# Optimization experiments

Measured on AMD Instinct MI355X. Metric: run time of the kernel, lower is better.

Reference implementation:

```python
import jax, jax.numpy as jnp
import numpy as np

B = 16384
S = 7
CELL = 1.0 / 7.0   # CELL_SILE
LC = 5.0           # lambda_coord
LN = 0.5           # lambda_noobj


def setup_inputs() -> dict:
    key = jax.random.key(0)
    k1, k2, k3 = jax.random.split(key, 3)
    predictions = jax.random.normal(k1, (B, S, S, 30), dtype=jnp.float32)
    targets = jax.random.uniform(k2, (B, S, S, 30), dtype=jnp.float32)
    # channel 4 is the objectness flag; code requires it to be exactly 0 or 1
    conf = (jax.random.uniform(k3, (B, S, S)) < 0.25).astype(jnp.float32)
    targets = targets.at[..., 4].set(conf)
    return {"predictions": predictions, "targets": targets}


def _box_corners(xy, wh):
    # Faithful to the original in-place bug: x2y2 uses the ALREADY-UPDATED x1y1
    xy1 = xy * CELL - wh * 0.5
    xy2 = xy1 * CELL + wh * 0.5
    return xy1, xy2


def _loss_terms(predictions, targets):
    p = predictions.reshape(-1, 30)   # [N, 30], N = B*S*S
    t = targets.reshape(-1, 30)
    obj = (t[:, 4] == 1.0).astype(p.dtype)
    noobj = (t[:, 4] == 0.0).astype(p.dtype)

    # no-object confidence loss on cols 4 and 9
    noobj_loss = LN * jnp.sum(noobj * (jnp.square(p[:, 4] - t[:, 4]) + jnp.square(p[:, 9] - t[:, 9])))

    # two predicted boxes per cell: cols 0:4 and 5:9 ; wh are sqrt-encoded -> square
    pb = jnp.stack([p[:, 0:4], p[:, 5:9]], axis=1)        # [N, 2, 4]
    pxy1, pxy2 = _box_corners(pb[..., 0:2], jnp.square(pb[..., 2:4]))  # [N,2,2]
    txy1, txy2 = _box_corners(t[:, None, 0:2], jnp.square(t[:, None, 2:4]))  # [N,1,2]

    # torchvision.ops.box_iou math (no clamp on areas, clamp(0) on intersection)
    lt = jnp.maximum(pxy1, txy1)
    rb = jnp.minimum(pxy2, txy2)
    inter = jnp.prod(jnp.clip(rb - lt, 0.0, None), axis=-1)   # [N, 2]
    area_p = jnp.prod(pxy2 - pxy1, axis=-1)                   # [N, 2]
    area_t = jnp.prod(txy2 - txy1, axis=-1)                   # [N, 1]
    iou = inter / (area_p + area_t - inter)                   # [N, 2]

    idx = jnp.argmax(iou, axis=1)                             # responsible box in {0,1}

    cols = idx[:, None] * 5 + jnp.arange(4)[None, :]          # [N, 4]
    cp = jnp.take_along_axis(p, cols, axis=1)
    ct = jnp.take_along_axis(t, cols, axis=1)
    center_loss = LC * jnp.sum(obj * jnp.sum(jnp.square(cp[:, 0:2] - ct[:, 0:2]), axis=1))
    wh_loss = LC * jnp.sum(obj * jnp.sum(jnp.square(cp[:, 2:4] - ct[:, 2:4]), axis=1))

    ccol = (idx * 5 + 4)[:, None]
    conf_loss = LC * jnp.sum(obj * jnp.square(jnp.take_along_axis(p, ccol, axis=1) - jnp.take_along_axis(t, ccol, axis=1))[:, 0])

    kcol = (jnp.argmax(t[:, 10:30], axis=1) + 10)[:, None]
    cls_loss = LC * jnp.sum(obj * jnp.square(jnp.take_along_axis(p, kcol, axis=1) - jnp.take_along_axis(t, kcol, axis=1))[:, 0])

    total = noobj_loss + center_loss + wh_loss + conf_loss + cls_loss
    return cls_loss, conf_loss, center_loss + wh_loss, total


def reference(predictions, targets):
    return _loss_terms(predictions, targets)
```

## Files before the change

### kernel.cpp

```cpp
#include <hip/hip_runtime.h>


constexpr int   WSZ  = 64;
constexpr int   NC   = 16384 * 7 * 7;
constexpr int   NT   = NC / WSZ;
constexpr int   GRID = 4096;
constexpr float CELL = 1.0f / 7.0f;
constexpr float LC   = 5.0f;
constexpr float LN   = 0.5f;

__launch_bounds__(WSZ, 4)
__global__ void yolo_partial(const float* __restrict__ P, const float* __restrict__ T,
                             float4* __restrict__ ws)
{
    __shared__ float sT[WSZ * 30];
    const int lane = threadIdx.x;
    float a_cls = 0.f, a_conf = 0.f, a_cw = 0.f, a_noobj = 0.f;

    for (int tile = blockIdx.x; tile < NT; tile += GRID) {
        const size_t base = (size_t)tile * (WSZ * 30);

        const float4* gT = reinterpret_cast<const float4*>(T + base);
        float4* s4 = reinterpret_cast<float4*>(sT);
        #pragma unroll
        for (int k = 0; k < 8; ++k) {
            int idx = k * WSZ + lane;
            if (idx < 480) s4[idx] = gT[idx];
        }

        const float* prow = P + base + (size_t)lane * 30;
        float pv[10];
        #pragma unroll
        for (int j = 0; j < 5; ++j) {
            float2 v = reinterpret_cast<const float2*>(prow)[j];
            pv[2 * j] = v.x; pv[2 * j + 1] = v.y;
        }
        __syncthreads();

        const float* tt = sT + lane * 30;
        float tv[30];
        #pragma unroll
        for (int j = 0; j < 15; ++j) {
            float2 v = reinterpret_cast<const float2*>(tt)[j];
            tv[2 * j] = v.x; tv[2 * j + 1] = v.y;
        }

        int kc = 10;
        float best = tv[10];
        #pragma unroll
        for (int k = 11; k < 30; ++k) {
            if (tv[k] > best) { best = tv[k]; kc = k; }
        }
        float2 pg = *reinterpret_cast<const float2*>(prow + (kc & ~1));
        float pk = (kc & 1) ? pg.y : pg.x;

        const float t4 = tv[4];
        const float obj   = (t4 == 1.0f) ? 1.0f : 0.0f;
        const float noobj = (t4 == 0.0f) ? 1.0f : 0.0f;

        float d4 = pv[4] - t4;
        float d9 = pv[9] - tv[9];
        a_noobj += noobj * (d4 * d4 + d9 * d9);

        float tw2 = tv[2] * tv[2], th2 = tv[3] * tv[3];
        float tx1 = tv[0] * CELL - 0.5f * tw2;
        float tx2 = tx1 * CELL + 0.5f * tw2;
        float ty1 = tv[1] * CELL - 0.5f * th2;
        float ty2 = ty1 * CELL + 0.5f * th2;
        float area_t = (tx2 - tx1) * (ty2 - ty1);

        float iou0, iou1;
        #pragma unroll
        for (int b = 0; b < 2; ++b) {
            float bw2 = pv[5 * b + 2] * pv[5 * b + 2];
            float bh2 = pv[5 * b + 3] * pv[5 * b + 3];
            float px1 = pv[5 * b + 0] * CELL - 0.5f * bw2;
            float px2 = px1 * CELL + 0.5f * bw2;
            float py1 = pv[5 * b + 1] * CELL - 0.5f * bh2;
            float py2 = py1 * CELL + 0.5f * bh2;
            float ltx = fmaxf(px1, tx1), lty = fmaxf(py1, ty1);
            float rbx = fminf(px2, tx2), rby = fminf(py2, ty2);
            float inter = fmaxf(rbx - ltx, 0.0f) * fmaxf(rby - lty, 0.0f);
            float area_p = (px2 - px1) * (py2 - py1);
            float iou = inter / (area_p + area_t - inter);
            if (b == 0) iou0 = iou; else iou1 = iou;
        }
        const bool b1 = (iou1 > iou0);

        float cpx = b1 ? pv[5] : pv[0], ctx = b1 ? tv[5] : tv[0];
        float cpy = b1 ? pv[6] : pv[1], cty = b1 ? tv[6] : tv[1];
        float cpw = b1 ? pv[7] : pv[2], ctw = b1 ? tv[7] : tv[2];
        float cph = b1 ? pv[8] : pv[3], cth = b1 ? tv[8] : tv[3];
        float cpc = b1 ? pv[9] : pv[4], ctc = b1 ? tv[9] : tv[4];

        float dx = cpx - ctx, dy = cpy - cty;
        float dw = cpw - ctw, dh = cph - cth;
        a_cw   += obj * (dx * dx + dy * dy + dw * dw + dh * dh);
        float dc = cpc - ctc;
        a_conf += obj * dc * dc;
        float dk = pk - best;
        a_cls  += obj * dk * dk;

        __syncthreads();
    }

    float vals[4] = { a_cls, a_conf, a_cw, a_noobj };
    #pragma unroll
    for (int c = 0; c < 4; ++c) {
        #pragma unroll
        for (int off = 32; off > 0; off >>= 1)
            vals[c] += __shfl_down(vals[c], off, 64);
    }
    if (lane == 0)
        ws[blockIdx.x] = make_float4(vals[0], vals[1], vals[2], vals[3]);
}

__launch_bounds__(1024, 1)
__global__ void yolo_reduce(const float4* __restrict__ ws, float* __restrict__ out)
{
    __shared__ float red[4][16];
    const int tid = threadIdx.x;

    float s0 = 0.f, s1 = 0.f, s2 = 0.f, s3 = 0.f;
    for (int b = tid; b < GRID; b += 1024) {
        float4 v = ws[b];
        s0 += v.x; s1 += v.y; s2 += v.z; s3 += v.w;
    }
    float vals[4] = { s0, s1, s2, s3 };
    #pragma unroll
    for (int c = 0; c < 4; ++c) {
        #pragma unroll
        for (int off = 32; off > 0; off >>= 1)
            vals[c] += __shfl_down(vals[c], off, 64);
        if ((tid & 63) == 0) red[c][tid >> 6] = vals[c];
    }
    __syncthreads();
    if (tid == 0) {
        float t0 = 0.f, t1 = 0.f, t2 = 0.f, t3 = 0.f;
        #pragma unroll
        for (int w = 0; w < 16; ++w) {
            t0 += red[0][w]; t1 += red[1][w]; t2 += red[2][w]; t3 += red[3][w];
        }
        out[0] = LC * t0;
        out[1] = LC * t1;
        out[2] = LC * t2;
        out[3] = LN * t3 + LC * (t0 + t1 + t2);
    }
}

extern "C" void kernel_launch(void* const* d_in, const int* in_sizes, int n_in,
                              void* d_out, int out_size, void* d_ws, size_t ws_size,
                              hipStream_t stream) {
    const float* P = (const float*)d_in[0];
    const float* T = (const float*)d_in[1];
    float* out = (float*)d_out;
    float4* ws = (float4*)d_ws;

    yolo_partial<<<GRID, WSZ, 0, stream>>>(P, T, ws);
    yolo_reduce<<<1, 1024, 0, stream>>>(ws, out);
}
```

Measured before the change: 207.3 us.

## Load two cells per thread with float4 loads and drop shared-memory staging

```diff
diff --git a/kernel.cpp b/kernel.cpp
--- a/kernel.cpp
+++ b/kernel.cpp
@@ -1,108 +1,106 @@
 #include <hip/hip_runtime.h>
 
 
-constexpr int   WSZ  = 64;
-constexpr int   NC   = 16384 * 7 * 7;
-constexpr int   NT   = NC / WSZ;
-constexpr int   GRID = 4096;
-constexpr float CELL = 1.0f / 7.0f;
-constexpr float LC   = 5.0f;
-constexpr float LN   = 0.5f;
+constexpr int   TPB   = 256;
+constexpr int   NC    = 16384 * 7 * 7;
+constexpr int   NPAIR = NC / 2;
+constexpr int   NBLK  = NPAIR / TPB;
+constexpr float CELL  = 1.0f / 7.0f;
+constexpr float LC    = 5.0f;
+constexpr float LN    = 0.5f;
 
-__launch_bounds__(WSZ, 4)
+__device__ __forceinline__ void cell_terms(const float* __restrict__ pv,
+                                           const float* __restrict__ tv,
+                                           float& a_cls, float& a_conf,
+                                           float& a_cw, float& a_noobj)
+{
+    const float t4 = tv[4];
+    const float obj   = (t4 == 1.0f) ? 1.0f : 0.0f;
+    const float noobj = (t4 == 0.0f) ? 1.0f : 0.0f;
+
+    float d4 = pv[4] - t4;
+    float d9 = pv[9] - tv[9];
+    a_noobj += noobj * (d4 * d4 + d9 * d9);
+
+    float tw2 = tv[2] * tv[2], th2 = tv[3] * tv[3];
+    float tx1 = tv[0] * CELL - 0.5f * tw2;
+    float tx2 = tx1 * CELL + 0.5f * tw2;
+    float ty1 = tv[1] * CELL - 0.5f * th2;
+    float ty2 = ty1 * CELL + 0.5f * th2;
+    float area_t = (tx2 - tx1) * (ty2 - ty1);
+
+    float iou0, iou1;
+    #pragma unroll
+    for (int b = 0; b < 2; ++b) {
+        float bw2 = pv[5 * b + 2] * pv[5 * b + 2];
+        float bh2 = pv[5 * b + 3] * pv[5 * b + 3];
+        float px1 = pv[5 * b + 0] * CELL - 0.5f * bw2;
+        float px2 = px1 * CELL + 0.5f * bw2;
+        float py1 = pv[5 * b + 1] * CELL - 0.5f * bh2;
+        float py2 = py1 * CELL + 0.5f * bh2;
+        float ltx = fmaxf(px1, tx1), lty = fmaxf(py1, ty1);
+        float rbx = fminf(px2, tx2), rby = fminf(py2, ty2);
+        float inter = fmaxf(rbx - ltx, 0.0f) * fmaxf(rby - lty, 0.0f);
+        float area_p = (px2 - px1) * (py2 - py1);
+        float iou = inter / (area_p + area_t - inter);
+        if (b == 0) iou0 = iou; else iou1 = iou;
+    }
+    const bool b1 = (iou1 > iou0);
+
+    float cpx = b1 ? pv[5] : pv[0], ctx = b1 ? tv[5] : tv[0];
+    float cpy = b1 ? pv[6] : pv[1], cty = b1 ? tv[6] : tv[1];
+    float cpw = b1 ? pv[7] : pv[2], ctw = b1 ? tv[7] : tv[2];
+    float cph = b1 ? pv[8] : pv[3], cth = b1 ? tv[8] : tv[3];
+    float cpc = b1 ? pv[9] : pv[4], ctc = b1 ? tv[9] : tv[4];
+
+    float dx = cpx - ctx, dy = cpy - cty;
+    float dw = cpw - ctw, dh = cph - cth;
+    a_cw   += obj * (dx * dx + dy * dy + dw * dw + dh * dh);
+    float dc = cpc - ctc;
+    a_conf += obj * dc * dc;
+
+    float best = tv[10];
+    float pk   = pv[10];
+    #pragma unroll
+    for (int k = 11; k < 30; ++k) {
+        bool gt = (tv[k] > best);
+        best = gt ? tv[k] : best;
+        pk   = gt ? pv[k] : pk;
+    }
+    float dk = pk - best;
+    a_cls += obj * dk * dk;
+}
+
+__launch_bounds__(TPB, 2)
 __global__ void yolo_partial(const float* __restrict__ P, const float* __restrict__ T,
                              float4* __restrict__ ws)
 {
-    __shared__ float sT[WSZ * 30];
-    const int lane = threadIdx.x;
+    __shared__ float red[4][TPB / 64];
+
+    const int tid  = threadIdx.x;
+    const int pair = blockIdx.x * TPB + tid;
+
+    const float4* p4 = reinterpret_cast<const float4*>(P + (size_t)pair * 60);
+    const float4* t4 = reinterpret_cast<const float4*>(T + (size_t)pair * 60);
+
+    float4 pr[15], tr[15];
+    #pragma unroll
+    for (int j = 0; j < 15; ++j) pr[j] = p4[j];
+    #pragma unroll
+    for (int j = 0; j < 15; ++j) tr[j] = t4[j];
+
+    float pv[60], tv[60];
+    #pragma unroll
+    for (int j = 0; j < 15; ++j) {
+        pv[4 * j + 0] = pr[j].x; pv[4 * j + 1] = pr[j].y;
+        pv[4 * j + 2] = pr[j].z; pv[4 * j + 3] = pr[j].w;
+        tv[4 * j + 0] = tr[j].x; tv[4 * j + 1] = tr[j].y;
+        tv[4 * j + 2] = tr[j].z; tv[4 * j + 3] = tr[j].w;
+    }
+
     float a_cls = 0.f, a_conf = 0.f, a_cw = 0.f, a_noobj = 0.f;
-
-    for (int tile = blockIdx.x; tile < NT; tile += GRID) {
-        const size_t base = (size_t)tile * (WSZ * 30);
-
-        const float4* gT = reinterpret_cast<const float4*>(T + base);
-        float4* s4 = reinterpret_cast<float4*>(sT);
-        #pragma unroll
-        for (int k = 0; k < 8; ++k) {
-            int idx = k * WSZ + lane;
-            if (idx < 480) s4[idx] = gT[idx];
-        }
-
-        const float* prow = P + base + (size_t)lane * 30;
-        float pv[10];
-        #pragma unroll
-        for (int j = 0; j < 5; ++j) {
-            float2 v = reinterpret_cast<const float2*>(prow)[j];
-            pv[2 * j] = v.x; pv[2 * j + 1] = v.y;
-        }
-        __syncthreads();
-
-        const float* tt = sT + lane * 30;
-        float tv[30];
-        #pragma unroll
-        for (int j = 0; j < 15; ++j) {
-            float2 v = reinterpret_cast<const float2*>(tt)[j];
-            tv[2 * j] = v.x; tv[2 * j + 1] = v.y;
-        }
-
-        int kc = 10;
-        float best = tv[10];
-        #pragma unroll
-        for (int k = 11; k < 30; ++k) {
-            if (tv[k] > best) { best = tv[k]; kc = k; }
-        }
-        float2 pg = *reinterpret_cast<const float2*>(prow + (kc & ~1));
-        float pk = (kc & 1) ? pg.y : pg.x;
-
-        const float t4 = tv[4];
-        const float obj   = (t4 == 1.0f) ? 1.0f : 0.0f;
-        const float noobj = (t4 == 0.0f) ? 1.0f : 0.0f;
-
-        float d4 = pv[4] - t4;
-        float d9 = pv[9] - tv[9];
-        a_noobj += noobj * (d4 * d4 + d9 * d9);
-
-        float tw2 = tv[2] * tv[2], th2 = tv[3] * tv[3];
-        float tx1 = tv[0] * CELL - 0.5f * tw2;
-        float tx2 = tx1 * CELL + 0.5f * tw2;
-        float ty1 = tv[1] * CELL - 0.5f * th2;
-        float ty2 = ty1 * CELL + 0.5f * th2;
-        float area_t = (tx2 - tx1) * (ty2 - ty1);
-
-        float iou0, iou1;
-        #pragma unroll
-        for (int b = 0; b < 2; ++b) {
-            float bw2 = pv[5 * b + 2] * pv[5 * b + 2];
-            float bh2 = pv[5 * b + 3] * pv[5 * b + 3];
-            float px1 = pv[5 * b + 0] * CELL - 0.5f * bw2;
-            float px2 = px1 * CELL + 0.5f * bw2;
-            float py1 = pv[5 * b + 1] * CELL - 0.5f * bh2;
-            float py2 = py1 * CELL + 0.5f * bh2;
-            float ltx = fmaxf(px1, tx1), lty = fmaxf(py1, ty1);
-            float rbx = fminf(px2, tx2), rby = fminf(py2, ty2);
-            float inter = fmaxf(rbx - ltx, 0.0f) * fmaxf(rby - lty, 0.0f);
-            float area_p = (px2 - px1) * (py2 - py1);
-            float iou = inter / (area_p + area_t - inter);
-            if (b == 0) iou0 = iou; else iou1 = iou;
-        }
-        const bool b1 = (iou1 > iou0);
-
-        float cpx = b1 ? pv[5] : pv[0], ctx = b1 ? tv[5] : tv[0];
-        float cpy = b1 ? pv[6] : pv[1], cty = b1 ? tv[6] : tv[1];
-        float cpw = b1 ? pv[7] : pv[2], ctw = b1 ? tv[7] : tv[2];
-        float cph = b1 ? pv[8] : pv[3], cth = b1 ? tv[8] : tv[3];
-        float cpc = b1 ? pv[9] : pv[4], ctc = b1 ? tv[9] : tv[4];
-
-        float dx = cpx - ctx, dy = cpy - cty;
-        float dw = cpw - ctw, dh = cph - cth;
-        a_cw   += obj * (dx * dx + dy * dy + dw * dw + dh * dh);
-        float dc = cpc - ctc;
-        a_conf += obj * dc * dc;
-        float dk = pk - best;
-        a_cls  += obj * dk * dk;
-
-        __syncthreads();
-    }
+    cell_terms(pv,      tv,      a_cls, a_conf, a_cw, a_noobj);
+    cell_terms(pv + 30, tv + 30, a_cls, a_conf, a_cw, a_noobj);
 
     float vals[4] = { a_cls, a_conf, a_cw, a_noobj };
     #pragma unroll
@@ -110,9 +108,17 @@
         #pragma unroll
         for (int off = 32; off > 0; off >>= 1)
             vals[c] += __shfl_down(vals[c], off, 64);
+        if ((tid & 63) == 0) red[c][tid >> 6] = vals[c];
     }
-    if (lane == 0)
-        ws[blockIdx.x] = make_float4(vals[0], vals[1], vals[2], vals[3]);
+    __syncthreads();
+    if (tid == 0) {
+        float4 s;
+        s.x = red[0][0] + red[0][1] + red[0][2] + red[0][3];
+        s.y = red[1][0] + red[1][1] + red[1][2] + red[1][3];
+        s.z = red[2][0] + red[2][1] + red[2][2] + red[2][3];
+        s.w = red[3][0] + red[3][1] + red[3][2] + red[3][3];
+        ws[blockIdx.x] = s;
+    }
 }
 
 __launch_bounds__(1024, 1)
@@ -122,7 +128,7 @@
     const int tid = threadIdx.x;
 
     float s0 = 0.f, s1 = 0.f, s2 = 0.f, s3 = 0.f;
-    for (int b = tid; b < GRID; b += 1024) {
+    for (int b = tid; b < NBLK; b += 1024) {
         float4 v = ws[b];
         s0 += v.x; s1 += v.y; s2 += v.z; s3 += v.w;
     }
@@ -156,6 +162,6 @@
     float* out = (float*)d_out;
     float4* ws = (float4*)d_ws;
 
-    yolo_partial<<<GRID, WSZ, 0, stream>>>(P, T, ws);
+    yolo_partial<<<NBLK, TPB, 0, stream>>>(P, T, ws);
     yolo_reduce<<<1, 1024, 0, stream>>>(ws, out);
 }
```

After: 249.5 us. 1.2x slower.
